# Kernel optimization log

Hardware: AMD Instinct MI355X
Metric: run time of the kernel (lower is better)

The kernel has to match this reference:

```python
import jax, jax.numpy as jnp
import numpy as np

TEMPERATURE = 0.1
MARGIN = 0.5
B, D = 8192, 128


def setup_inputs() -> dict:
    key = jax.random.key(0)
    k1, k2 = jax.random.split(key)
    z1 = jax.random.normal(k1, (B, D), dtype=jnp.float32)
    z2 = jax.random.normal(k2, (B, D), dtype=jnp.float32)
    return {"z1": z1, "z2": z2}


def _normalize(x):
    # F.normalize(x, dim=-1): x / max(||x||, eps) with eps=1e-12
    n = jnp.linalg.norm(x, axis=-1, keepdims=True)
    return x / jnp.maximum(n, 1e-12)


def reference(z1, z2):
    z1 = _normalize(z1)
    z2 = _normalize(z2)
    b = z1.shape[0]
    pos_sim = jnp.sum(z1 * z2, axis=-1)                      # [B]
    z_all = jnp.concatenate([z1, z2], axis=0)                # [2B, D]
    neg_sim = (z_all @ z_all.T) / TEMPERATURE                # [2B, 2B]
    idx = jnp.arange(b)
    neg_inf = jnp.asarray(-jnp.inf, neg_sim.dtype)
    # mask the (i, B+i) and (B+i, i) positive pairs
    neg_sim = neg_sim.at[idx, idx + b].set(neg_inf)
    neg_sim = neg_sim.at[idx + b, idx].set(neg_inf)
    hardest_neg = jnp.max(neg_sim, axis=-1)                  # [2B]
    pos_full = jnp.concatenate([pos_sim, pos_sim])           # [2B]
    loss = jax.nn.relu(hardest_neg + MARGIN - pos_full)
    return jnp.mean(loss)
```

## Files before the change

kernel.cpp:

```cpp
#include <hip/hip_runtime.h>


constexpr int   kB      = 8192;
constexpr int   kD      = 128;
constexpr float kInvT   = 10.0f;
constexpr float kMargin = 0.5f;
constexpr int   kBlocks = 512;

__global__ __launch_bounds__(256) void hncl_partial(const float* __restrict__ z1,
                                                    const float* __restrict__ z2,
                                                    float* __restrict__ ws) {
    const int lane        = threadIdx.x & 63;
    const int sub         = lane & 31;
    const int half        = lane >> 5;
    const int wave_in_blk = threadIdx.x >> 6;
    const int gwave       = blockIdx.x * 4 + wave_in_blk;

    float local = 0.0f;

    #pragma unroll
    for (int iter = 0; iter < 2; ++iter) {
        const int row = gwave * 2 + half + iter * (kB / 2);
        const float4 a = reinterpret_cast<const float4*>(z1 + (size_t)row * kD)[sub];
        const float4 b = reinterpret_cast<const float4*>(z2 + (size_t)row * kD)[sub];

        float d11 = a.x * a.x + a.y * a.y + a.z * a.z + a.w * a.w;
        float d22 = b.x * b.x + b.y * b.y + b.z * b.z + b.w * b.w;
        float d12 = a.x * b.x + a.y * b.y + a.z * b.z + a.w * b.w;

        #pragma unroll
        for (int off = 16; off > 0; off >>= 1) {
            d11 += __shfl_down(d11, off, 32);
            d22 += __shfl_down(d22, off, 32);
            d12 += __shfl_down(d12, off, 32);
        }

        if (sub == 0) {
            const float n1 = fmaxf(sqrtf(d11), 1e-12f);
            const float n2 = fmaxf(sqrtf(d22), 1e-12f);
            const float pos = d12 / (n1 * n2);
            const float s1  = d11 / (n1 * n1);
            const float s2  = d22 / (n2 * n2);
            local += fmaxf(s1 * kInvT + kMargin - pos, 0.0f)
                   + fmaxf(s2 * kInvT + kMargin - pos, 0.0f);
        }
    }

    __shared__ float wsum[8];
    if (sub == 0) wsum[wave_in_blk * 2 + half] = local;
    __syncthreads();
    if (threadIdx.x == 0) {
        float s = 0.0f;
        #pragma unroll
        for (int i = 0; i < 8; ++i) s += wsum[i];
        ws[blockIdx.x] = s;
    }
}

__global__ __launch_bounds__(256) void hncl_final(const float* __restrict__ ws,
                                                  float* __restrict__ out) {
    const int lane = threadIdx.x & 63;
    const int wave = threadIdx.x >> 6;

    const float2 p = reinterpret_cast<const float2*>(ws)[threadIdx.x];
    float v = p.x + p.y;
    #pragma unroll
    for (int off = 32; off > 0; off >>= 1) v += __shfl_down(v, off, 64);

    __shared__ float wsum[4];
    if (lane == 0) wsum[wave] = v;
    __syncthreads();
    if (threadIdx.x == 0) {
        out[0] = (wsum[0] + wsum[1] + wsum[2] + wsum[3]) * (1.0f / (2.0f * (float)kB));
    }
}

extern "C" void kernel_launch(void* const* d_in, const int* in_sizes, int n_in,
                              void* d_out, int out_size, void* d_ws, size_t ws_size,
                              hipStream_t stream) {
    const float* z1 = reinterpret_cast<const float*>(d_in[0]);
    const float* z2 = reinterpret_cast<const float*>(d_in[1]);
    float* ws  = reinterpret_cast<float*>(d_ws);
    float* out = reinterpret_cast<float*>(d_out);

    hncl_partial<<<kBlocks, 256, 0, stream>>>(z1, z2, ws);
    hncl_final<<<1, 256, 0, stream>>>(ws, out);
}
```

Measured before the change: 59.92 us.

## Fuse partial and final reductions into one cooperative kernel with grid sync

Merges the per-block partial reduction and the final reduction into a single kernel launched cooperatively. A grid-wide sync sits between them, and block 0 then sums the partials. Block count is halved, and each thread loads four rows of both inputs before doing any arithmetic, to put more memory loads in flight. This removes the second kernel launch, at the cost of cooperative-launch overhead and a grid barrier.

```diff
diff --git a/kernel.cpp b/kernel.cpp
--- a/kernel.cpp
+++ b/kernel.cpp
@@ -1,32 +1,41 @@
 #include <hip/hip_runtime.h>
+#include <hip/hip_cooperative_groups.h>
+
+namespace cg = cooperative_groups;
 
 
-constexpr int   kB      = 8192;
-constexpr int   kD      = 128;
-constexpr float kInvT   = 10.0f;
-constexpr float kMargin = 0.5f;
-constexpr int   kBlocks = 512;
+constexpr int   kB       = 8192;
+constexpr int   kD       = 128;
+constexpr float kInvT    = 10.0f;
+constexpr float kMargin  = 0.5f;
+constexpr int   kBlocks  = 256;
+constexpr int   kThreads = 256;
+constexpr int   kIters   = 4;
 
-__global__ __launch_bounds__(256) void hncl_partial(const float* __restrict__ z1,
-                                                    const float* __restrict__ z2,
-                                                    float* __restrict__ ws) {
+__global__ __launch_bounds__(kThreads) void hncl_fused(const float* __restrict__ z1,
+                                                       const float* __restrict__ z2,
+                                                       float* __restrict__ ws,
+                                                       float* __restrict__ out) {
     const int lane        = threadIdx.x & 63;
     const int sub         = lane & 31;
     const int half        = lane >> 5;
     const int wave_in_blk = threadIdx.x >> 6;
     const int gwave       = blockIdx.x * 4 + wave_in_blk;
 
+    float4 a[kIters], b[kIters];
+    #pragma unroll
+    for (int it = 0; it < kIters; ++it) {
+        const int row = gwave * 2 + half + it * (kB / kIters);
+        a[it] = reinterpret_cast<const float4*>(z1 + (size_t)row * kD)[sub];
+        b[it] = reinterpret_cast<const float4*>(z2 + (size_t)row * kD)[sub];
+    }
+
     float local = 0.0f;
-
     #pragma unroll
-    for (int iter = 0; iter < 2; ++iter) {
-        const int row = gwave * 2 + half + iter * (kB / 2);
-        const float4 a = reinterpret_cast<const float4*>(z1 + (size_t)row * kD)[sub];
-        const float4 b = reinterpret_cast<const float4*>(z2 + (size_t)row * kD)[sub];
-
-        float d11 = a.x * a.x + a.y * a.y + a.z * a.z + a.w * a.w;
-        float d22 = b.x * b.x + b.y * b.y + b.z * b.z + b.w * b.w;
-        float d12 = a.x * b.x + a.y * b.y + a.z * b.z + a.w * b.w;
+    for (int it = 0; it < kIters; ++it) {
+        float d11 = a[it].x * a[it].x + a[it].y * a[it].y + a[it].z * a[it].z + a[it].w * a[it].w;
+        float d22 = b[it].x * b[it].x + b[it].y * b[it].y + b[it].z * b[it].z + b[it].w * b[it].w;
+        float d12 = a[it].x * b[it].x + a[it].y * b[it].y + a[it].z * b[it].z + a[it].w * b[it].w;
 
         #pragma unroll
         for (int off = 16; off > 0; off >>= 1) {
@@ -55,23 +64,20 @@
         for (int i = 0; i < 8; ++i) s += wsum[i];
         ws[blockIdx.x] = s;
     }
-}
 
-__global__ __launch_bounds__(256) void hncl_final(const float* __restrict__ ws,
-                                                  float* __restrict__ out) {
-    const int lane = threadIdx.x & 63;
-    const int wave = threadIdx.x >> 6;
+    cg::this_grid().sync();
 
-    const float2 p = reinterpret_cast<const float2*>(ws)[threadIdx.x];
-    float v = p.x + p.y;
-    #pragma unroll
-    for (int off = 32; off > 0; off >>= 1) v += __shfl_down(v, off, 64);
+    if (blockIdx.x == 0) {
+        float v = ws[threadIdx.x];
+        #pragma unroll
+        for (int off = 32; off > 0; off >>= 1) v += __shfl_down(v, off, 64);
 
-    __shared__ float wsum[4];
-    if (lane == 0) wsum[wave] = v;
-    __syncthreads();
-    if (threadIdx.x == 0) {
-        out[0] = (wsum[0] + wsum[1] + wsum[2] + wsum[3]) * (1.0f / (2.0f * (float)kB));
+        __shared__ float fsum[4];
+        if (lane == 0) fsum[wave_in_blk] = v;
+        __syncthreads();
+        if (threadIdx.x == 0) {
+            out[0] = (fsum[0] + fsum[1] + fsum[2] + fsum[3]) * (1.0f / (2.0f * (float)kB));
+        }
     }
 }
 
@@ -83,6 +89,7 @@
     float* ws  = reinterpret_cast<float*>(d_ws);
     float* out = reinterpret_cast<float*>(d_out);
 
-    hncl_partial<<<kBlocks, 256, 0, stream>>>(z1, z2, ws);
-    hncl_final<<<1, 256, 0, stream>>>(ws, out);
+    void* args[] = {(void*)&z1, (void*)&z2, (void*)&ws, (void*)&out};
+    hipLaunchCooperativeKernel(reinterpret_cast<const void*>(hncl_fused),
+                               dim3(kBlocks), dim3(kThreads), args, 0, stream);
 }
```

Result: slower. 95.37 us (+59.2%).
